# Kernel tuning notes

Hardware: AMD Instinct MI355X
Metric: run time of the kernel (lower is better)

The kernel has to match this reference:

```python
import jax, jax.numpy as jnp
import numpy as np

DIM = 512; NHEAD = 8; DHEAD = 64; INNER = NHEAD * DHEAD
CTX = 1024; NOCT = int(np.ceil(np.log2(CTX))) + 1  # 11
B = 8; SEQ = 256; MEM = 768


def positional_encoding(ctx, num_oct):
    # matches Attention.positional_encoding on coords=arange(ctx).view(ctx,1),
    # start_octave = 1 - num_oct
    coords = jnp.arange(ctx, dtype=jnp.float32)[:, None, None]        # (ctx,1,1)
    octaves = jnp.arange(1 - num_oct, 1, dtype=jnp.float32)           # (num_oct,)
    mult = (2.0 ** octaves) * np.pi
    scaled = (coords * mult).reshape(ctx, num_oct)                    # (ctx, num_oct)
    return jnp.concatenate([jnp.sin(scaled), jnp.cos(scaled)], axis=-1)  # (ctx, 2*num_oct)


def get_shifts(mem, seq, ctx):
    coords = jnp.arange(mem + seq - 1, -1, -1) - (seq - 1)            # (mem+seq,)
    shifts = coords[None, :] + jnp.arange(seq)[:, None]               # (seq, mem+seq)
    oob = (shifts < 0) | (shifts > ctx - 1)
    bias = jnp.where(oob, -jnp.inf, 0.0).astype(jnp.float32)
    return jnp.clip(shifts, 0, ctx - 1), bias


def setup_inputs() -> dict:
    key = jax.random.key(0)
    ks = jax.random.split(key, 8)
    s = 0.02
    return {
        "x": jax.random.normal(ks[0], (B, SEQ, DIM), jnp.float32),
        "memory": jax.random.normal(ks[1], (B, MEM, DIM), jnp.float32),
        "W_qkv": jax.random.normal(ks[2], (DIM, 3 * INNER), jnp.float32) * s,
        "W_rel": jax.random.normal(ks[3], (2 * NOCT, INNER), jnp.float32) * s,
        "W_out": jax.random.normal(ks[4], (INNER, DIM), jnp.float32) * s,
        "b_out": jnp.zeros((DIM,), jnp.float32),
        "u_emb": jax.random.normal(ks[5], (DHEAD,), jnp.float32),
        "v_emb": jax.random.normal(ks[6], (DHEAD,), jnp.float32),
    }


def reference(x, memory, W_qkv, W_rel, W_out, b_out, u_emb, v_emb):
    b, seq, _ = x.shape
    mem = memory.shape[1]
    total = mem + seq
    scale = DHEAD ** -0.5

    shifts, bias = get_shifts(mem, seq, CTX)                          # (seq,total) each
    R = positional_encoding(CTX, NOCT)                                # (CTX, 2*NOCT)
    kr = (R @ W_rel)[shifts].reshape(seq, total, NHEAD, DHEAD)        # n m h d

    qkv = jnp.concatenate([memory, x], axis=1) @ W_qkv                # (b,total,3*INNER)
    q, k, v = jnp.split(qkv, 3, axis=-1)

    def heads(t):
        return t.reshape(b, total, NHEAD, DHEAD).transpose(0, 2, 1, 3)  # b h m d

    q = heads(q)[:, :, mem:]                                          # b h n d (queries only over x)
    k = heads(k)
    v = heads(v)

    term_a = jnp.einsum('bhnd,bhmd->bhnm', q, k)
    term_b = jnp.einsum('bhnd,nmhd->bhnm', q, kr)
    term_c = jnp.einsum('d,bhmd->bhm', u_emb, k)[:, :, None, :]        # broadcast over n
    term_d = jnp.einsum('d,nmhd->hnm', v_emb, kr)[None]                # broadcast over b

    dots = (term_a + term_b + term_c + term_d) * scale + bias          # banded -inf mask
    attn = jax.nn.softmax(dots, axis=-1)                               # dropout p=0 -> identity
    out = jnp.einsum('bhnm,bhmd->bnhd', attn, v).reshape(b, seq, INNER)
    return out @ W_out + b_out
```

## Files before the change

kernel.cpp:

```cpp
#include <hip/hip_runtime.h>
#include <hip/hip_bf16.h>
#include <math.h>

typedef unsigned short u16;
typedef unsigned int u32;
typedef __attribute__((ext_vector_type(8))) short short8;
typedef __attribute__((ext_vector_type(4))) float floatx4;

constexpr int kB     = 8;
constexpr int kSEQ   = 256;
constexpr int kMEM   = 768;
constexpr int kTOTAL = 1024;

__device__ __forceinline__ float bf2f(u16 u) {
  return __uint_as_float(((u32)u) << 16);
}
__device__ __forceinline__ u16 f2bf(float f) {
  __hip_bfloat16 h = __float2bfloat16(f);
  return *reinterpret_cast<u16*>(&h);
}
__device__ __forceinline__ void gload_lds16(const u16* g, u16* l) {
  __builtin_amdgcn_global_load_lds(
      (__attribute__((address_space(1))) const unsigned int*)g,
      (__attribute__((address_space(3))) unsigned int*)l, 16, 0, 0);
}

__device__ __forceinline__ void wtconv_body(
    const float* __restrict__ W, u16* __restrict__ Wt, int K, int N,
    int n0, int k0, int tid, float (*tile)[65])
{
  int r = tid >> 4, c4 = (tid & 15) * 4;
#pragma unroll
  for (int v = 0; v < 4; v++) {
    float4 w4 = *(const float4*)(W + (size_t)(k0 + v * 16 + r) * N + n0 + c4);
    tile[v * 16 + r][c4 + 0] = w4.x;
    tile[v * 16 + r][c4 + 1] = w4.y;
    tile[v * 16 + r][c4 + 2] = w4.z;
    tile[v * 16 + r][c4 + 3] = w4.w;
  }
  __syncthreads();
#pragma unroll
  for (int v = 0; v < 4; v++) {
    int rn = v * 16 + r;
    ushort4 o;
    o.x = f2bf(tile[c4 + 0][rn]);
    o.y = f2bf(tile[c4 + 1][rn]);
    o.z = f2bf(tile[c4 + 2][rn]);
    o.w = f2bf(tile[c4 + 3][rn]);
    *(ushort4*)(Wt + (size_t)(n0 + rn) * K + k0 + c4) = o;
  }
}

__global__ __launch_bounds__(256) void prep_kernel(
    const float* __restrict__ x, const float* __restrict__ memf,
    const float* __restrict__ W_qkv, const float* __restrict__ W_out,
    const float* __restrict__ W_rel, const float* __restrict__ v_emb,
    const float* __restrict__ u_emb,
    u16* __restrict__ Xb, u16* __restrict__ WqkvT, u16* __restrict__ WoutT,
    u16* __restrict__ Rrel_bf, float* __restrict__ vR)
{
  __shared__ float tile[64][65];
  __shared__ float pe[22];
  __shared__ float prod[512];
  int bid = blockIdx.x;
  int t = threadIdx.x;
  if (bid < 1024) {
    int s = bid;
    if (t < 22) {
      int o = (t < 11) ? t : (t - 11);
      float mult = ldexpf(3.14159265358979323846f, o - 10);
      float ang = (float)s * mult;
      pe[t] = (t < 11) ? sinf(ang) : cosf(ang);
    }
    __syncthreads();
#pragma unroll
    for (int c = 0; c < 2; c++) {
      int j = t + c * 256;
      float acc = 0.f;
#pragma unroll
      for (int o = 0; o < 22; ++o) acc += pe[o] * W_rel[o * 512 + j];
      u16 rbf = f2bf(acc);
      Rrel_bf[(size_t)s * 512 + j] = rbf;
      prod[j] = acc * v_emb[j & 63] - bf2f(rbf) * u_emb[j & 63];
    }
    __syncthreads();
    if (t < 8) {
      float a = 0.f;
#pragma unroll 8
      for (int d = 0; d < 64; d++) a += prod[t * 64 + d];
      vR[t * 1024 + s] = a * 0.125f;
    }
  } else if (bid < 3072) {
    int idx = (bid - 1024) * 256 + t;
    int row = idx >> 6, c8 = idx & 63;
    int b = row >> 10, pos = row & 1023;
    const float* src = (pos < kMEM)
        ? memf + (size_t)(b * kMEM + pos) * 512
        : x    + (size_t)(b * kSEQ + pos - kMEM) * 512;
    const float4* s4 = (const float4*)(src + c8 * 8);
    float4 a = s4[0], bb = s4[1];
    u16 tmp[8] = {f2bf(a.x),  f2bf(a.y),  f2bf(a.z),  f2bf(a.w),
                  f2bf(bb.x), f2bf(bb.y), f2bf(bb.z), f2bf(bb.w)};
    *(uint4*)(Xb + (size_t)row * 512 + c8 * 8) = *(uint4*)tmp;
  } else if (bid < 3264) {
    int r = bid - 3072;
    wtconv_body(W_qkv, WqkvT, 512, 1536, (r % 24) * 64, (r / 24) * 64, t, tile);
  } else {
    int r = bid - 3264;
    wtconv_body(W_out, WoutT, 512, 512, (r % 8) * 64, (r / 8) * 64, t, tile);
  }
}

__global__ __launch_bounds__(256) void gemm_bf16(
    const u16* __restrict__ A, const u16* __restrict__ Bt,
    int lda, int ldb, int ksteps,
    u16* __restrict__ Cbf, int ldc, int qscale, const float* __restrict__ uq)
{
  __shared__ u16 As[128 * 64];
  __shared__ u16 Bs[128 * 64];
  int tid = threadIdx.x;
  int id = blockIdx.y * gridDim.x + blockIdx.x;
  int gy = gridDim.y;
  int bm = (id % gy) * 128, bn = (id / gy) * 128;
  int ln = tid & 15, quad = (tid >> 4) & 3, w = tid >> 6;
  int moff = (w >> 1) * 64, noff = (w & 1) * 64;
  int l7 = ln & 7;
  floatx4 acc[4][4];
#pragma unroll
  for (int mi = 0; mi < 4; mi++)
#pragma unroll
    for (int ni = 0; ni < 4; ni++) acc[mi][ni] = (floatx4){0.f, 0.f, 0.f, 0.f};

  int srow[4], sgch[4];
#pragma unroll
  for (int v = 0; v < 4; v++) {
    int f = v * 256 + tid;
    srow[v] = f >> 3;
    sgch[v] = (f & 7) ^ ((f >> 3) & 7);
  }

  for (int ks = 0; ks < ksteps; ks++) {
    int k0 = ks * 64;
#pragma unroll
    for (int v = 0; v < 4; v++) {
      gload_lds16(A + (size_t)(bm + srow[v]) * lda + k0 + sgch[v] * 8,
                  &As[(v * 256 + tid) * 8]);
      gload_lds16(Bt + (size_t)(bn + srow[v]) * ldb + k0 + sgch[v] * 8,
                  &Bs[(v * 256 + tid) * 8]);
    }
    __syncthreads();
#pragma unroll
    for (int kb = 0; kb < 2; kb++) {
      short8 af[4], bfr[4];
#pragma unroll
      for (int mi = 0; mi < 4; mi++) {
        int row = moff + mi * 16 + ln;
        af[mi] = *(const short8*)&As[row * 64 + (((quad + 4 * kb) ^ l7) << 3)];
      }
#pragma unroll
      for (int ni = 0; ni < 4; ni++) {
        int row = noff + ni * 16 + ln;
        bfr[ni] = *(const short8*)&Bs[row * 64 + (((quad + 4 * kb) ^ l7) << 3)];
      }
#pragma unroll
      for (int mi = 0; mi < 4; mi++)
#pragma unroll
        for (int ni = 0; ni < 4; ni++)
          acc[mi][ni] = __builtin_amdgcn_mfma_f32_16x16x32_bf16(
              af[mi], bfr[ni], acc[mi][ni], 0, 0, 0);
    }
    __syncthreads();
  }

  int r0 = bm + moff + quad * 4;
#pragma unroll
  for (int ni = 0; ni < 4; ni++) {
    int col = bn + noff + ni * 16 + ln;
    bool isq = qscale && col < 512;
    float scale = isq ? 0.125f : 1.f;
    float uadd = isq ? uq[col & 63] : 0.f;
#pragma unroll
    for (int mi = 0; mi < 4; mi++) {
#pragma unroll
      for (int r = 0; r < 4; r++) {
        int row = r0 + mi * 16 + r;
        Cbf[(size_t)row * ldc + col] = f2bf((acc[mi][ni][r] + uadd) * scale);
      }
    }
  }
}

__global__ __launch_bounds__(256) void gemm_bf16_64(
    const u16* __restrict__ A, const u16* __restrict__ Bt,
    int lda, int ldb, int ksteps,
    float* __restrict__ Cf, int ldc, const float* __restrict__ bias)
{
  __shared__ u16 As[64 * 64];
  __shared__ u16 Bs[64 * 64];
  int tid = threadIdx.x;
  int id = blockIdx.y * gridDim.x + blockIdx.x;
  int gy = gridDim.y;
  int bm = (id % gy) * 64, bn = (id / gy) * 64;
  int ln = tid & 15, quad = (tid >> 4) & 3, w = tid >> 6;
  int moff = (w >> 1) * 32, noff = (w & 1) * 32;
  int l7 = ln & 7;
  floatx4 acc[2][2];
#pragma unroll
  for (int mi = 0; mi < 2; mi++)
#pragma unroll
    for (int ni = 0; ni < 2; ni++) acc[mi][ni] = (floatx4){0.f, 0.f, 0.f, 0.f};

  int srow[2], sgch[2];
#pragma unroll
  for (int v = 0; v < 2; v++) {
    int f = v * 256 + tid;
    srow[v] = f >> 3;
    sgch[v] = (f & 7) ^ ((f >> 3) & 7);
  }

  for (int ks = 0; ks < ksteps; ks++) {
    int k0 = ks * 64;
#pragma unroll
    for (int v = 0; v < 2; v++) {
      gload_lds16(A + (size_t)(bm + srow[v]) * lda + k0 + sgch[v] * 8,
                  &As[(v * 256 + tid) * 8]);
      gload_lds16(Bt + (size_t)(bn + srow[v]) * ldb + k0 + sgch[v] * 8,
                  &Bs[(v * 256 + tid) * 8]);
    }
    __syncthreads();
#pragma unroll
    for (int kb = 0; kb < 2; kb++) {
      short8 af[2], bfr[2];
#pragma unroll
      for (int mi = 0; mi < 2; mi++) {
        int row = moff + mi * 16 + ln;
        af[mi] = *(const short8*)&As[row * 64 + (((quad + 4 * kb) ^ l7) << 3)];
      }
#pragma unroll
      for (int ni = 0; ni < 2; ni++) {
        int row = noff + ni * 16 + ln;
        bfr[ni] = *(const short8*)&Bs[row * 64 + (((quad + 4 * kb) ^ l7) << 3)];
      }
#pragma unroll
      for (int mi = 0; mi < 2; mi++)
#pragma unroll
        for (int ni = 0; ni < 2; ni++)
          acc[mi][ni] = __builtin_amdgcn_mfma_f32_16x16x32_bf16(
              af[mi], bfr[ni], acc[mi][ni], 0, 0, 0);
    }
    __syncthreads();
  }

  int r0 = bm + moff + quad * 4;
#pragma unroll
  for (int ni = 0; ni < 2; ni++) {
    int col = bn + noff + ni * 16 + ln;
    float cv = bias[col];
#pragma unroll
    for (int mi = 0; mi < 2; mi++) {
#pragma unroll
      for (int r = 0; r < 4; r++) {
        int row = r0 + mi * 16 + r;
        Cf[(size_t)row * ldc + col] = acc[mi][ni][r] + cv;
      }
    }
  }
}

__global__ __launch_bounds__(256) void attn_mfma(
    const u16* __restrict__ qkv_bf, const u16* __restrict__ Rrel_bf,
    const float* __restrict__ vR,
    u16* __restrict__ Opart, float* __restrict__ lbuf)
{
  constexpr int LD = 72;
  __shared__ u16 Vt[2][64 * LD];
  __shared__ u16 Ps[64 * LD];

  int nt = blockIdx.x >> 3, p = blockIdx.x & 7;
  int h = blockIdx.y, b = blockIdx.z;
  int n0 = nt * 64, bh = b * 8 + h;
  int tid = threadIdx.x;
  int w = tid >> 6, lane = tid & 63;
  int l15 = lane & 15, quad = lane >> 4, q8 = quad * 8;

  int sr0 = tid >> 3, sc8 = tid & 7;
  int sr1 = (256 + tid) >> 3;
  int vg0 = ((sr0 >> 3) ^ sc8) * 8 + (sr0 & 7);
  int vg1 = ((sr1 >> 3) ^ sc8) * 8 + (sr1 & 7);

  const u16* qrow = qkv_bf + (size_t)(b * kTOTAL + kMEM + n0 + 16 * w + l15) * 1536 + h * 64;
  short8 qf0 = *(const short8*)(qrow + q8);
  short8 qf1 = *(const short8*)(qrow + 32 + q8);

  int bidx[4];
#pragma unroll
  for (int r = 0; r < 4; r++) {
    int il = 4 * quad + r;
    bidx[r] = ((quad << 4) | ((il + 15 - l15) & 15)) << 2;
  }

  const u16* kpart = qkv_bf + (size_t)(b * kTOTAL) * 1536 + 512 + h * 64;
  const float* vRh = vR + h * 1024;

  int ntiles = 13 + nt;
  int mtA = p, mtB = p + 8;
  bool hasB = (mtB < ntiles);
  bool lastB = (mtB == ntiles - 1);

  {
    const u16* va = kpart + (size_t)mtA * 64 * 1536 + 512;
    const u16* vb = kpart + (size_t)mtB * 64 * 1536 + 512;
    uint4 a0 = *(const uint4*)(va + (size_t)sr0 * 1536 + sc8 * 8);
    uint4 a1 = *(const uint4*)(va + (size_t)sr1 * 1536 + sc8 * 8);
    uint4 b0 = *(const uint4*)(vb + (size_t)sr0 * 1536 + sc8 * 8);
    uint4 b1 = *(const uint4*)(vb + (size_t)sr1 * 1536 + sc8 * 8);
    const u16* pa0v = (const u16*)&a0;
    const u16* pa1v = (const u16*)&a1;
    const u16* pb0v = (const u16*)&b0;
    const u16* pb1v = (const u16*)&b1;
#pragma unroll
    for (int i = 0; i < 8; i++) {
      Vt[0][(sc8 * 8 + i) * LD + vg0] = pa0v[i];
      Vt[0][(sc8 * 8 + i) * LD + vg1] = pa1v[i];
      Vt[1][(sc8 * 8 + i) * LD + vg0] = pb0v[i];
      Vt[1][(sc8 * 8 + i) * LD + vg1] = pb1v[i];
    }
  }
  __syncthreads();

  floatx4 o_acc[4];
  float l_i[4];
#pragma unroll
  for (int r = 0; r < 4; r++) l_i[r] = 0.f;
#pragma unroll
  for (int nd = 0; nd < 4; nd++) o_acc[nd] = (floatx4){0.f, 0.f, 0.f, 0.f};

  int s_base_w = kMEM + n0 + 16 * w;

  auto tile_body = [&](int mt, bool lastt, const u16* VtX) {
    int m0 = mt * 64;
    const u16* kbase = kpart + (size_t)m0 * 1536;
    int sb = s_base_w - m0;

    short8 kb0[4], kb1[4];
#pragma unroll
    for (int ni = 0; ni < 4; ni++) {
      const u16* kr = kbase + (size_t)(16 * ni + l15) * 1536;
      kb0[ni] = *(const short8*)(kr + q8);
      kb1[ni] = *(const short8*)(kr + 32 + q8);
    }

    float tf[5][4];
#pragma unroll
    for (int ct = 0; ct < 5; ct++) {
      int s = sb - 63 + 16 * ct + l15;
      s = min(max(s, 0), 1023);
      const u16* rr = Rrel_bf + (size_t)s * 512 + h * 64;
      short8 rb0 = *(const short8*)(rr + q8);
      short8 rb1 = *(const short8*)(rr + 32 + q8);
      float vv = vRh[s];
      floatx4 t = (floatx4){0.f, 0.f, 0.f, 0.f};
      t = __builtin_amdgcn_mfma_f32_16x16x32_bf16(qf0, rb0, t, 0, 0, 0);
      t = __builtin_amdgcn_mfma_f32_16x16x32_bf16(qf1, rb1, t, 0, 0, 0);
#pragma unroll
      for (int r = 0; r < 4; r++) tf[ct][r] = t[r] + vv;
    }

    float tsh[4][4];
#pragma unroll
    for (int ni = 0; ni < 4; ni++) {
#pragma unroll
      for (int r = 0; r < 4; r++) {
        int il = 4 * quad + r;
        float tv = (l15 < il) ? tf[4 - ni][r] : tf[3 - ni][r];
        tsh[ni][r] = __int_as_float(
            __builtin_amdgcn_ds_bpermute(bidx[r], __float_as_int(tv)));
      }
    }

    floatx4 sa[4];
#pragma unroll
    for (int ni = 0; ni < 4; ni++) {
      floatx4 s4 = (floatx4){0.f, 0.f, 0.f, 0.f};
      s4 = __builtin_amdgcn_mfma_f32_16x16x32_bf16(qf0, kb0[ni], s4, 0, 0, 0);
      s4 = __builtin_amdgcn_mfma_f32_16x16x32_bf16(qf1, kb1[ni], s4, 0, 0, 0);
      sa[ni] = s4;
    }

#pragma unroll
    for (int ni = 0; ni < 4; ni++) {
#pragma unroll
      for (int r = 0; r < 4; r++) {
        int il = 4 * quad + r;
        float val = sa[ni][r] + tsh[ni][r];
        if (lastt && (16 * ni + l15) > (16 * w + il)) val = -1e30f;
        float e = __expf(val);
        l_i[r] += e;
        int prow = 16 * w + il;
        Ps[prow * LD + (l15 & 7) + (((2 * ni + (l15 >> 3)) ^ (prow >> 3)) << 3)] =
            f2bf(e);
      }
    }

    int rowq = 16 * w + l15, rr3q = rowq >> 3;
    short8 pa0 = *(const short8*)&Ps[rowq * LD + ((quad ^ rr3q) << 3)];
    short8 pa1 = *(const short8*)&Ps[rowq * LD + (((quad + 4) ^ rr3q) << 3)];
#pragma unroll
    for (int nd = 0; nd < 4; nd++) {
      int rowv = 16 * nd + l15, rr3v = rowv >> 3;
      short8 vb0 = *(const short8*)&VtX[rowv * LD + ((quad ^ rr3v) << 3)];
      short8 vb1 = *(const short8*)&VtX[rowv * LD + (((quad + 4) ^ rr3v) << 3)];
      o_acc[nd] = __builtin_amdgcn_mfma_f32_16x16x32_bf16(pa0, vb0, o_acc[nd], 0, 0, 0);
      o_acc[nd] = __builtin_amdgcn_mfma_f32_16x16x32_bf16(pa1, vb1, o_acc[nd], 0, 0, 0);
    }
  };

  tile_body(mtA, false, Vt[0]);
  if (hasB) tile_body(mtB, lastB, Vt[1]);

  int pbase = (p * 64 + bh) * 256;
#pragma unroll
  for (int r = 0; r < 4; r++) {
    float l = l_i[r];
#pragma unroll
    for (int off = 1; off < 16; off <<= 1)
      l += __shfl_xor(l, off, 64);
    int n = n0 + 16 * w + 4 * quad + r;
    u16* orow = Opart + ((size_t)(pbase + n) << 6) + l15;
#pragma unroll
    for (int nd = 0; nd < 4; nd++)
      orow[16 * nd] = f2bf(o_acc[nd][r]);
    if (l15 == 0) lbuf[pbase + n] = l;
  }
}

__global__ __launch_bounds__(256) void attn_combine(
    const u16* __restrict__ Opart, const float* __restrict__ lbuf,
    u16* __restrict__ aout_bf)
{
  int idx = blockIdx.x * 256 + threadIdx.x;
  int bh = idx >> 12, n = (idx >> 4) & 255, d4 = idx & 15;
  int rowi = bh * 256 + n;
  float den = 0.f;
  float num[4] = {0.f, 0.f, 0.f, 0.f};
#pragma unroll
  for (int p = 0; p < 8; p++) {
    den += lbuf[(p << 14) + rowi];
    uint2 raw = *(const uint2*)(Opart + (((size_t)(p << 14) + rowi) << 6) + d4 * 4);
    const u16* us = (const u16*)&raw;
#pragma unroll
    for (int j = 0; j < 4; j++) num[j] += bf2f(us[j]);
  }
  float inv = 1.f / den;
  int b = bh >> 3, h = bh & 7;
  ushort4 o;
  o.x = f2bf(num[0] * inv);
  o.y = f2bf(num[1] * inv);
  o.z = f2bf(num[2] * inv);
  o.w = f2bf(num[3] * inv);
  *(ushort4*)(aout_bf + (size_t)(b * kSEQ + n) * 512 + h * 64 + d4 * 4) = o;
}

extern "C" void kernel_launch(void* const* d_in, const int* in_sizes, int n_in,
                              void* d_out, int out_size, void* d_ws, size_t ws_size,
                              hipStream_t stream) {
  (void)in_sizes; (void)n_in; (void)out_size; (void)ws_size;
  const float* x      = (const float*)d_in[0];
  const float* memory = (const float*)d_in[1];
  const float* W_qkv  = (const float*)d_in[2];
  const float* W_rel  = (const float*)d_in[3];
  const float* W_out  = (const float*)d_in[4];
  const float* b_out  = (const float*)d_in[5];
  const float* u_emb  = (const float*)d_in[6];
  const float* v_emb  = (const float*)d_in[7];
  float* out = (float*)d_out;

  char* ws = (char*)d_ws;
  u16*   qkv_bf  = (u16*)ws;                         ws += (size_t)12582912 * 2;
  u16*   Xcat_bf = (u16*)ws;                         ws += (size_t)4194304 * 2;
  u16*   aout_bf = (u16*)ws;                         ws += (size_t)1048576 * 2;
  u16*   Opart   = (u16*)ws;                         ws += (size_t)8388608 * 2;
  float* lbuf    = (float*)ws;                       ws += (size_t)131072 * 4;
  u16*   WqkvT   = (u16*)ws;                         ws += (size_t)786432 * 2;
  u16*   WoutT   = (u16*)ws;                         ws += (size_t)262144 * 2;
  u16*   Rrel_bf = (u16*)ws;                         ws += (size_t)524288 * 2;
  float* vR      = (float*)ws;                       ws += (size_t)8192 * 4;

  prep_kernel<<<3328, 256, 0, stream>>>(
      x, memory, W_qkv, W_out, W_rel, v_emb, u_emb,
      Xcat_bf, WqkvT, WoutT, Rrel_bf, vR);

  gemm_bf16<<<dim3(12, 64), 256, 0, stream>>>(
      Xcat_bf, WqkvT, 512, 512, 8, qkv_bf, 1536, 1, u_emb);

  attn_mfma<<<dim3(32, 8, 8), 256, 0, stream>>>(
      qkv_bf, Rrel_bf, vR, Opart, lbuf);

  attn_combine<<<1024, 256, 0, stream>>>(Opart, lbuf, aout_bf);

  gemm_bf16_64<<<dim3(8, 32), 256, 0, stream>>>(
      aout_bf, WoutT, 512, 512, 8, out, 512, b_out);
}
```

Measured before the change: 157.7 us.

## Software-pipeline attention tile loads and interleave two tile computations

Moves the K, Rrel and vR global loads for the first tile ahead of the V-transpose barrier. The second tile's loads are prefetched while the first tile's relative-position and QK MFMAs run. The per-tile lambda is split into stages, and the two tiles' work is interleaved to hide global memory latency. The hasB/lastB branching is replaced by an always-applied positional causal mask. Blocks whose second tile lies past the causal limit now compute it fully masked, which is wasted work, and more live registers may reduce occupancy.

```diff
diff --git a/kernel.cpp b/kernel.cpp
--- a/kernel.cpp
+++ b/kernel.cpp
@@ -288,10 +288,45 @@
   int vg0 = ((sr0 >> 3) ^ sc8) * 8 + (sr0 & 7);
   int vg1 = ((sr1 >> 3) ^ sc8) * 8 + (sr1 & 7);
 
+  const u16* kpart = qkv_bf + (size_t)(b * kTOTAL) * 1536 + 512 + h * 64;
+  const float* vRh = vR + h * 1024;
+
+  int mtA = p, mtB = p + 8;
+  int m0A = mtA * 64, m0B = mtB * 64;
+  int s_base_w = kMEM + n0 + 16 * w;
+  int sbA = s_base_w - m0A, sbB = s_base_w - m0B;
+
+  const u16* va = kpart + (size_t)mtA * 64 * 1536 + 512;
+  const u16* vb = kpart + (size_t)mtB * 64 * 1536 + 512;
+  uint4 a0 = *(const uint4*)(va + (size_t)sr0 * 1536 + sc8 * 8);
+  uint4 a1 = *(const uint4*)(va + (size_t)sr1 * 1536 + sc8 * 8);
+  uint4 b0 = *(const uint4*)(vb + (size_t)sr0 * 1536 + sc8 * 8);
+  uint4 b1 = *(const uint4*)(vb + (size_t)sr1 * 1536 + sc8 * 8);
+
   const u16* qrow = qkv_bf + (size_t)(b * kTOTAL + kMEM + n0 + 16 * w + l15) * 1536 + h * 64;
   short8 qf0 = *(const short8*)(qrow + q8);
   short8 qf1 = *(const short8*)(qrow + 32 + q8);
 
+  short8 kbA0[4], kbA1[4];
+#pragma unroll
+  for (int ni = 0; ni < 4; ni++) {
+    const u16* kr = kpart + (size_t)(m0A + 16 * ni + l15) * 1536;
+    kbA0[ni] = *(const short8*)(kr + q8);
+    kbA1[ni] = *(const short8*)(kr + 32 + q8);
+  }
+
+  short8 rbA0[5], rbA1[5];
+  float vRcA[5];
+#pragma unroll
+  for (int ct = 0; ct < 5; ct++) {
+    int s = sbA - 63 + 16 * ct + l15;
+    s = min(max(s, 0), 1023);
+    const u16* rr = Rrel_bf + (size_t)s * 512 + h * 64;
+    rbA0[ct] = *(const short8*)(rr + q8);
+    rbA1[ct] = *(const short8*)(rr + 32 + q8);
+    vRcA[ct] = vRh[s];
+  }
+
   int bidx[4];
 #pragma unroll
   for (int r = 0; r < 4; r++) {
@@ -299,21 +334,7 @@
     bidx[r] = ((quad << 4) | ((il + 15 - l15) & 15)) << 2;
   }
 
-  const u16* kpart = qkv_bf + (size_t)(b * kTOTAL) * 1536 + 512 + h * 64;
-  const float* vRh = vR + h * 1024;
-
-  int ntiles = 13 + nt;
-  int mtA = p, mtB = p + 8;
-  bool hasB = (mtB < ntiles);
-  bool lastB = (mtB == ntiles - 1);
-
   {
-    const u16* va = kpart + (size_t)mtA * 64 * 1536 + 512;
-    const u16* vb = kpart + (size_t)mtB * 64 * 1536 + 512;
-    uint4 a0 = *(const uint4*)(va + (size_t)sr0 * 1536 + sc8 * 8);
-    uint4 a1 = *(const uint4*)(va + (size_t)sr1 * 1536 + sc8 * 8);
-    uint4 b0 = *(const uint4*)(vb + (size_t)sr0 * 1536 + sc8 * 8);
-    uint4 b1 = *(const uint4*)(vb + (size_t)sr1 * 1536 + sc8 * 8);
     const u16* pa0v = (const u16*)&a0;
     const u16* pa1v = (const u16*)&a1;
     const u16* pb0v = (const u16*)&b0;
@@ -335,38 +356,18 @@
 #pragma unroll
   for (int nd = 0; nd < 4; nd++) o_acc[nd] = (floatx4){0.f, 0.f, 0.f, 0.f};
 
-  int s_base_w = kMEM + n0 + 16 * w;
-
-  auto tile_body = [&](int mt, bool lastt, const u16* VtX) {
-    int m0 = mt * 64;
-    const u16* kbase = kpart + (size_t)m0 * 1536;
-    int sb = s_base_w - m0;
-
-    short8 kb0[4], kb1[4];
-#pragma unroll
-    for (int ni = 0; ni < 4; ni++) {
-      const u16* kr = kbase + (size_t)(16 * ni + l15) * 1536;
-      kb0[ni] = *(const short8*)(kr + q8);
-      kb1[ni] = *(const short8*)(kr + 32 + q8);
-    }
-
-    float tf[5][4];
+  auto do_T = [&](short8 (&rb0)[5], short8 (&rb1)[5], float (&vRc)[5],
+                  float (&tf)[5][4]) {
 #pragma unroll
     for (int ct = 0; ct < 5; ct++) {
-      int s = sb - 63 + 16 * ct + l15;
-      s = min(max(s, 0), 1023);
-      const u16* rr = Rrel_bf + (size_t)s * 512 + h * 64;
-      short8 rb0 = *(const short8*)(rr + q8);
-      short8 rb1 = *(const short8*)(rr + 32 + q8);
-      float vv = vRh[s];
       floatx4 t = (floatx4){0.f, 0.f, 0.f, 0.f};
-      t = __builtin_amdgcn_mfma_f32_16x16x32_bf16(qf0, rb0, t, 0, 0, 0);
-      t = __builtin_amdgcn_mfma_f32_16x16x32_bf16(qf1, rb1, t, 0, 0, 0);
-#pragma unroll
-      for (int r = 0; r < 4; r++) tf[ct][r] = t[r] + vv;
-    }
-
-    float tsh[4][4];
+      t = __builtin_amdgcn_mfma_f32_16x16x32_bf16(qf0, rb0[ct], t, 0, 0, 0);
+      t = __builtin_amdgcn_mfma_f32_16x16x32_bf16(qf1, rb1[ct], t, 0, 0, 0);
+#pragma unroll
+      for (int r = 0; r < 4; r++) tf[ct][r] = t[r] + vRc[ct];
+    }
+  };
+  auto do_tsh = [&](float (&tf)[5][4], float (&tsh)[4][4]) {
 #pragma unroll
     for (int ni = 0; ni < 4; ni++) {
 #pragma unroll
@@ -377,8 +378,8 @@
             __builtin_amdgcn_ds_bpermute(bidx[r], __float_as_int(tv)));
       }
     }
-
-    floatx4 sa[4];
+  };
+  auto do_QK = [&](short8 (&kb0)[4], short8 (&kb1)[4], floatx4 (&sa)[4]) {
 #pragma unroll
     for (int ni = 0; ni < 4; ni++) {
       floatx4 s4 = (floatx4){0.f, 0.f, 0.f, 0.f};
@@ -386,14 +387,15 @@
       s4 = __builtin_amdgcn_mfma_f32_16x16x32_bf16(qf1, kb1[ni], s4, 0, 0, 0);
       sa[ni] = s4;
     }
-
+  };
+  auto do_logits = [&](floatx4 (&sa)[4], float (&tsh)[4][4], int sb) {
 #pragma unroll
     for (int ni = 0; ni < 4; ni++) {
 #pragma unroll
       for (int r = 0; r < 4; r++) {
         int il = 4 * quad + r;
         float val = sa[ni][r] + tsh[ni][r];
-        if (lastt && (16 * ni + l15) > (16 * w + il)) val = -1e30f;
+        if ((16 * ni + l15) > (sb + il)) val = -1e30f;
         float e = __expf(val);
         l_i[r] += e;
         int prow = 16 * w + il;
@@ -401,7 +403,8 @@
             f2bf(e);
       }
     }
-
+  };
+  auto do_PV = [&](const u16* VtX) {
     int rowq = 16 * w + l15, rr3q = rowq >> 3;
     short8 pa0 = *(const short8*)&Ps[rowq * LD + ((quad ^ rr3q) << 3)];
     short8 pa1 = *(const short8*)&Ps[rowq * LD + (((quad + 4) ^ rr3q) << 3)];
@@ -415,8 +418,46 @@
     }
   };
 
-  tile_body(mtA, false, Vt[0]);
-  if (hasB) tile_body(mtB, lastB, Vt[1]);
+  float tfA[5][4];
+  do_T(rbA0, rbA1, vRcA, tfA);
+  float tshA[4][4];
+  do_tsh(tfA, tshA);
+
+  short8 rbB0[5], rbB1[5];
+  float vRcB[5];
+#pragma unroll
+  for (int ct = 0; ct < 5; ct++) {
+    int s = sbB - 63 + 16 * ct + l15;
+    s = min(max(s, 0), 1023);
+    const u16* rr = Rrel_bf + (size_t)s * 512 + h * 64;
+    rbB0[ct] = *(const short8*)(rr + q8);
+    rbB1[ct] = *(const short8*)(rr + 32 + q8);
+    vRcB[ct] = vRh[s];
+  }
+
+  floatx4 saA[4];
+  do_QK(kbA0, kbA1, saA);
+  do_logits(saA, tshA, sbA);
+
+  short8 kbB0[4], kbB1[4];
+#pragma unroll
+  for (int ni = 0; ni < 4; ni++) {
+    const u16* kr = kpart + (size_t)(m0B + 16 * ni + l15) * 1536;
+    kbB0[ni] = *(const short8*)(kr + q8);
+    kbB1[ni] = *(const short8*)(kr + 32 + q8);
+  }
+
+  float tfB[5][4];
+  do_T(rbB0, rbB1, vRcB, tfB);
+  float tshB[4][4];
+  do_tsh(tfB, tshB);
+
+  do_PV(Vt[0]);
+
+  floatx4 saB[4];
+  do_QK(kbB0, kbB1, saB);
+  do_logits(saB, tshB, sbB);
+  do_PV(Vt[1]);
 
   int pbase = (p * 64 + bh) * 256;
 #pragma unroll
```

Result: faster. 153.1 us (-2.9%).

## Pipeline attention over two key partitions and skip unused memory-row Q projection

Applied to the files above, without the earlier changes.

The attention kernel now splits the key range into 2 partitions per (head, query tile) instead of 8, giving each block 8 key tiles. Loads are software-pipelined: V is double-buffered in LDS, and the next tiles' K and relative-position rows are prefetched into registers while the current tile's MFMAs run. Masking is computed per tile from the relative offset, so fully masked tiles are processed but contribute nothing. This cuts the partial-output buffer and combine work by 4x, at the cost of far fewer blocks (512) and higher register and LDS use. Separately, the QKV GEMM skips blocks that would compute Q for memory rows, since those queries are never used.

```diff
diff --git a/kernel.cpp b/kernel.cpp
--- a/kernel.cpp
+++ b/kernel.cpp
@@ -122,6 +122,7 @@
   int id = blockIdx.y * gridDim.x + blockIdx.x;
   int gy = gridDim.y;
   int bm = (id % gy) * 128, bn = (id / gy) * 128;
+  if (qscale && bn < 512 && ((bm >> 7) & 7) < 6) return;
   int ln = tid & 15, quad = (tid >> 4) & 3, w = tid >> 6;
   int moff = (w >> 1) * 64, noff = (w & 1) * 64;
   int l7 = ln & 7;
@@ -273,11 +274,12 @@
     u16* __restrict__ Opart, float* __restrict__ lbuf)
 {
   constexpr int LD = 72;
-  __shared__ u16 Vt[2][64 * LD];
+  __shared__ u16 Vt[4][64 * LD];
   __shared__ u16 Ps[64 * LD];
 
-  int nt = blockIdx.x >> 3, p = blockIdx.x & 7;
-  int h = blockIdx.y, b = blockIdx.z;
+  int h = blockIdx.x;
+  int nt = blockIdx.y >> 1, p = blockIdx.y & 1;
+  int b = blockIdx.z;
   int n0 = nt * 64, bh = b * 8 + h;
   int tid = threadIdx.x;
   int w = tid >> 6, lane = tid & 63;
@@ -288,6 +290,10 @@
   int vg0 = ((sr0 >> 3) ^ sc8) * 8 + (sr0 & 7);
   int vg1 = ((sr1 >> 3) ^ sc8) * 8 + (sr1 & 7);
 
+  const u16* kpart = qkv_bf + (size_t)(b * kTOTAL) * 1536 + 512 + h * 64;
+  const float* vRh = vR + h * 1024;
+  int s_base_w = kMEM + n0 + 16 * w;
+
   const u16* qrow = qkv_bf + (size_t)(b * kTOTAL + kMEM + n0 + 16 * w + l15) * 1536 + h * 64;
   short8 qf0 = *(const short8*)(qrow + q8);
   short8 qf1 = *(const short8*)(qrow + 32 + q8);
@@ -299,74 +305,66 @@
     bidx[r] = ((quad << 4) | ((il + 15 - l15) & 15)) << 2;
   }
 
-  const u16* kpart = qkv_bf + (size_t)(b * kTOTAL) * 1536 + 512 + h * 64;
-  const float* vRh = vR + h * 1024;
-
-  int ntiles = 13 + nt;
-  int mtA = p, mtB = p + 8;
-  bool hasB = (mtB < ntiles);
-  bool lastB = (mtB == ntiles - 1);
-
-  {
-    const u16* va = kpart + (size_t)mtA * 64 * 1536 + 512;
-    const u16* vb = kpart + (size_t)mtB * 64 * 1536 + 512;
-    uint4 a0 = *(const uint4*)(va + (size_t)sr0 * 1536 + sc8 * 8);
-    uint4 a1 = *(const uint4*)(va + (size_t)sr1 * 1536 + sc8 * 8);
-    uint4 b0 = *(const uint4*)(vb + (size_t)sr0 * 1536 + sc8 * 8);
-    uint4 b1 = *(const uint4*)(vb + (size_t)sr1 * 1536 + sc8 * 8);
-    const u16* pa0v = (const u16*)&a0;
-    const u16* pa1v = (const u16*)&a1;
-    const u16* pb0v = (const u16*)&b0;
-    const u16* pb1v = (const u16*)&b1;
+  auto load_V = [&](int mtu, int mtv, uint4 (&vr)[4]) {
+    const u16* va = kpart + (size_t)mtu * 64 * 1536 + 512;
+    const u16* vb = kpart + (size_t)mtv * 64 * 1536 + 512;
+    vr[0] = *(const uint4*)(va + (size_t)sr0 * 1536 + sc8 * 8);
+    vr[1] = *(const uint4*)(va + (size_t)sr1 * 1536 + sc8 * 8);
+    vr[2] = *(const uint4*)(vb + (size_t)sr0 * 1536 + sc8 * 8);
+    vr[3] = *(const uint4*)(vb + (size_t)sr1 * 1536 + sc8 * 8);
+  };
+  auto write_V = [&](uint4 (&vr)[4], u16* bu, u16* bv) {
+    const u16* c0 = (const u16*)&vr[0];
+    const u16* c1 = (const u16*)&vr[1];
+    const u16* c2 = (const u16*)&vr[2];
+    const u16* c3 = (const u16*)&vr[3];
 #pragma unroll
     for (int i = 0; i < 8; i++) {
-      Vt[0][(sc8 * 8 + i) * LD + vg0] = pa0v[i];
-      Vt[0][(sc8 * 8 + i) * LD + vg1] = pa1v[i];
-      Vt[1][(sc8 * 8 + i) * LD + vg0] = pb0v[i];
-      Vt[1][(sc8 * 8 + i) * LD + vg1] = pb1v[i];
-    }
-  }
-  __syncthreads();
-
-  floatx4 o_acc[4];
-  float l_i[4];
-#pragma unroll
-  for (int r = 0; r < 4; r++) l_i[r] = 0.f;
-#pragma unroll
-  for (int nd = 0; nd < 4; nd++) o_acc[nd] = (floatx4){0.f, 0.f, 0.f, 0.f};
-
-  int s_base_w = kMEM + n0 + 16 * w;
-
-  auto tile_body = [&](int mt, bool lastt, const u16* VtX) {
-    int m0 = mt * 64;
-    const u16* kbase = kpart + (size_t)m0 * 1536;
-    int sb = s_base_w - m0;
-
-    short8 kb0[4], kb1[4];
+      bu[(sc8 * 8 + i) * LD + vg0] = c0[i];
+      bu[(sc8 * 8 + i) * LD + vg1] = c1[i];
+      bv[(sc8 * 8 + i) * LD + vg0] = c2[i];
+      bv[(sc8 * 8 + i) * LD + vg1] = c3[i];
+    }
+  };
+  auto load_K = [&](int mt, short8 (&k0)[4], short8 (&k1)[4]) {
 #pragma unroll
     for (int ni = 0; ni < 4; ni++) {
-      const u16* kr = kbase + (size_t)(16 * ni + l15) * 1536;
-      kb0[ni] = *(const short8*)(kr + q8);
-      kb1[ni] = *(const short8*)(kr + 32 + q8);
-    }
-
-    float tf[5][4];
+      const u16* kr = kpart + (size_t)(mt * 64 + 16 * ni + l15) * 1536;
+      k0[ni] = *(const short8*)(kr + q8);
+      k1[ni] = *(const short8*)(kr + 32 + q8);
+    }
+  };
+  auto load_R = [&](int sb, short8 (&r0)[5], short8 (&r1)[5], float (&vc)[5]) {
 #pragma unroll
     for (int ct = 0; ct < 5; ct++) {
       int s = sb - 63 + 16 * ct + l15;
       s = min(max(s, 0), 1023);
       const u16* rr = Rrel_bf + (size_t)s * 512 + h * 64;
-      short8 rb0 = *(const short8*)(rr + q8);
-      short8 rb1 = *(const short8*)(rr + 32 + q8);
-      float vv = vRh[s];
+      r0[ct] = *(const short8*)(rr + q8);
+      r1[ct] = *(const short8*)(rr + 32 + q8);
+      vc[ct] = vRh[s];
+    }
+  };
+
+  floatx4 o_acc[4];
+  float l_i[4];
+#pragma unroll
+  for (int r = 0; r < 4; r++) l_i[r] = 0.f;
+#pragma unroll
+  for (int nd = 0; nd < 4; nd++) o_acc[nd] = (floatx4){0.f, 0.f, 0.f, 0.f};
+
+  auto do_T = [&](short8 (&rb0)[5], short8 (&rb1)[5], float (&vRc)[5],
+                  float (&tf)[5][4]) {
+#pragma unroll
+    for (int ct = 0; ct < 5; ct++) {
       floatx4 t = (floatx4){0.f, 0.f, 0.f, 0.f};
-      t = __builtin_amdgcn_mfma_f32_16x16x32_bf16(qf0, rb0, t, 0, 0, 0);
-      t = __builtin_amdgcn_mfma_f32_16x16x32_bf16(qf1, rb1, t, 0, 0, 0);
-#pragma unroll
-      for (int r = 0; r < 4; r++) tf[ct][r] = t[r] + vv;
-    }
-
-    float tsh[4][4];
+      t = __builtin_amdgcn_mfma_f32_16x16x32_bf16(qf0, rb0[ct], t, 0, 0, 0);
+      t = __builtin_amdgcn_mfma_f32_16x16x32_bf16(qf1, rb1[ct], t, 0, 0, 0);
+#pragma unroll
+      for (int r = 0; r < 4; r++) tf[ct][r] = t[r] + vRc[ct];
+    }
+  };
+  auto do_tsh = [&](float (&tf)[5][4], float (&tsh)[4][4]) {
 #pragma unroll
     for (int ni = 0; ni < 4; ni++) {
 #pragma unroll
@@ -377,8 +375,8 @@
             __builtin_amdgcn_ds_bpermute(bidx[r], __float_as_int(tv)));
       }
     }
-
-    floatx4 sa[4];
+  };
+  auto do_QK = [&](short8 (&kb0)[4], short8 (&kb1)[4], floatx4 (&sa)[4]) {
 #pragma unroll
     for (int ni = 0; ni < 4; ni++) {
       floatx4 s4 = (floatx4){0.f, 0.f, 0.f, 0.f};
@@ -386,14 +384,15 @@
       s4 = __builtin_amdgcn_mfma_f32_16x16x32_bf16(qf1, kb1[ni], s4, 0, 0, 0);
       sa[ni] = s4;
     }
-
+  };
+  auto do_logits = [&](floatx4 (&sa)[4], float (&tsh)[4][4], int sb) {
 #pragma unroll
     for (int ni = 0; ni < 4; ni++) {
 #pragma unroll
       for (int r = 0; r < 4; r++) {
         int il = 4 * quad + r;
         float val = sa[ni][r] + tsh[ni][r];
-        if (lastt && (16 * ni + l15) > (16 * w + il)) val = -1e30f;
+        if ((16 * ni + l15) > (sb + il)) val = -1e30f;
         float e = __expf(val);
         l_i[r] += e;
         int prow = 16 * w + il;
@@ -401,7 +400,8 @@
             f2bf(e);
       }
     }
-
+  };
+  auto do_PV = [&](const u16* VtX) {
     int rowq = 16 * w + l15, rr3q = rowq >> 3;
     short8 pa0 = *(const short8*)&Ps[rowq * LD + ((quad ^ rr3q) << 3)];
     short8 pa1 = *(const short8*)&Ps[rowq * LD + (((quad + 4) ^ rr3q) << 3)];
@@ -415,8 +415,57 @@
     }
   };
 
-  tile_body(mtA, false, Vt[0]);
-  if (hasB) tile_body(mtB, lastB, Vt[1]);
+  uint4 vsl[2][4];
+  short8 rbP0[2][5], rbP1[2][5];
+  float vRcP[2][5];
+  load_V(p, p + 2, vsl[0]);
+  write_V(vsl[0], Vt[0], Vt[1]);
+  load_V(p + 4, p + 6, vsl[1]);
+  load_R(s_base_w - 64 * p, rbP0[0], rbP1[0], vRcP[0]);
+  __syncthreads();
+
+#pragma unroll
+  for (int g = 0; g < 4; g++) {
+    int mtU = p + 4 * g, mtV = p + 4 * g + 2;
+    int sbU = s_base_w - 64 * mtU, sbV = s_base_w - 64 * mtV;
+
+    if (g < 3) write_V(vsl[(g + 1) & 1], Vt[2 * ((g + 1) & 1)], Vt[2 * ((g + 1) & 1) + 1]);
+    if (g < 2) load_V(p + 4 * g + 8, p + 4 * g + 10, vsl[g & 1]);
+
+    short8 kbU0[4], kbU1[4];
+    load_K(mtU, kbU0, kbU1);
+
+    float tfU[5][4], tshU[4][4];
+    do_T(rbP0[g & 1], rbP1[g & 1], vRcP[g & 1], tfU);
+    do_tsh(tfU, tshU);
+
+    short8 rbV0[5], rbV1[5];
+    float vRcV[5];
+    load_R(sbV, rbV0, rbV1, vRcV);
+
+    floatx4 saU[4];
+    do_QK(kbU0, kbU1, saU);
+    do_logits(saU, tshU, sbU);
+
+    short8 kbV0[4], kbV1[4];
+    load_K(mtV, kbV0, kbV1);
+    if (g < 3)
+      load_R(s_base_w - 64 * (p + 4 * (g + 1)),
+             rbP0[(g + 1) & 1], rbP1[(g + 1) & 1], vRcP[(g + 1) & 1]);
+
+    float tfV[5][4], tshV[4][4];
+    do_T(rbV0, rbV1, vRcV, tfV);
+    do_tsh(tfV, tshV);
+
+    do_PV(Vt[2 * (g & 1)]);
+
+    floatx4 saV[4];
+    do_QK(kbV0, kbV1, saV);
+    do_logits(saV, tshV, sbV);
+    do_PV(Vt[2 * (g & 1) + 1]);
+
+    if (g < 3) __syncthreads();
+  }
 
   int pbase = (p * 64 + bh) * 256;
 #pragma unroll
@@ -444,7 +493,7 @@
   float den = 0.f;
   float num[4] = {0.f, 0.f, 0.f, 0.f};
 #pragma unroll
-  for (int p = 0; p < 8; p++) {
+  for (int p = 0; p < 2; p++) {
     den += lbuf[(p << 14) + rowi];
     uint2 raw = *(const uint2*)(Opart + (((size_t)(p << 14) + rowi) << 6) + d4 * 4);
     const u16* us = (const u16*)&raw;
@@ -479,8 +528,8 @@
   u16*   qkv_bf  = (u16*)ws;                         ws += (size_t)12582912 * 2;
   u16*   Xcat_bf = (u16*)ws;                         ws += (size_t)4194304 * 2;
   u16*   aout_bf = (u16*)ws;                         ws += (size_t)1048576 * 2;
-  u16*   Opart   = (u16*)ws;                         ws += (size_t)8388608 * 2;
-  float* lbuf    = (float*)ws;                       ws += (size_t)131072 * 4;
+  u16*   Opart   = (u16*)ws;                         ws += (size_t)2097152 * 2;
+  float* lbuf    = (float*)ws;                       ws += (size_t)32768 * 4;
   u16*   WqkvT   = (u16*)ws;                         ws += (size_t)786432 * 2;
   u16*   WoutT   = (u16*)ws;                         ws += (size_t)262144 * 2;
   u16*   Rrel_bf = (u16*)ws;                         ws += (size_t)524288 * 2;
@@ -493,7 +542,7 @@
   gemm_bf16<<<dim3(12, 64), 256, 0, stream>>>(
       Xcat_bf, WqkvT, 512, 512, 8, qkv_bf, 1536, 1, u_emb);
 
-  attn_mfma<<<dim3(32, 8, 8), 256, 0, stream>>>(
+  attn_mfma<<<dim3(8, 8, 8), 256, 0, stream>>>(
       qkv_bf, Rrel_bf, vR, Opart, lbuf);
 
   attn_combine<<<1024, 256, 0, stream>>>(Opart, lbuf, aout_bf);
```

After: 155.6 us. No clear change (-1.3%).
